# Kernel optimization log

Measured on AMD Instinct MI355X. Metric: run time of the kernel, lower is better.

Reference implementation:

```python
import jax, jax.numpy as jnp
import numpy as np

# Config constants from init_kwargs
DIM_GROUPS = [32, 32]   # hyper_cuts_dim_groups (sum == lsh_key_dim == d_key)
K_MAX = 64              # max candidates kept per query token


def _group_exact_match(qb, kb):
    """qb, kb: [B, L, d] binary {0,1} floats.
    Returns eq[b, i, j] = True iff all d bits of query i equal key j.
    Faithful to merge(Wu-Manber prefix match, Trie full-stride match):
    the Trie stores the full binary vector chunked by stride, so a Trie hit
    requires exact equality of the whole group's bit vector, which subsumes
    the Wu-Manber prefix condition; their intersection is exact equality.
    """
    # number of mismatching bits between query i and key j
    mism = (jnp.einsum('bid,bjd->bij', qb, 1.0 - kb)
            + jnp.einsum('bid,bjd->bij', 1.0 - qb, kb))
    return mism == 0.0


def setup_inputs() -> dict:
    key = jax.random.key(0)
    k1, k2 = jax.random.split(key)
    B, L, D = 4, 2048, 64
    return {
        'query_up': jax.random.normal(k1, (B, L, D), dtype=jnp.float32),
        'key_up': jax.random.normal(k2, (B, L, D), dtype=jnp.float32),
        'head_idx': 0,
    }


def reference(query_up, key_up, head_idx):
    B, L, _ = query_up.shape
    # binary_quantize: (x > 0).float()
    qb = (query_up > 0).astype(jnp.float32)
    kb = (key_up > 0).astype(jnp.float32)
    # per dim-group exact match (Wu-Manber \cap Trie), union across groups
    match = jnp.zeros((B, L, L), dtype=bool)
    start = 0
    for gd in DIM_GROUPS:
        match = match | _group_exact_match(qb[..., start:start + gd],
                                           kb[..., start:start + gd])
        start += gd
    # gather up to K_MAX smallest matching key indices per query, pad with -1
    idx = jnp.where(match, jnp.arange(L, dtype=jnp.int32)[None, None, :], L)
    cand = jnp.sort(idx, axis=-1)[..., :K_MAX]          # [B, L, K_MAX]
    return jnp.where(cand == L, -1, cand)
```

## Files before the change

kernel.cpp:

```cpp
#include <hip/hip_runtime.h>
#include <stdint.h>


#define LSEQ 2048
#define DDIM 64
#define KMAX 64
#define RPW  8
#define MQPB 32

__global__ __launch_bounds__(256) void sig_kernel(
    const float* __restrict__ key, uint2* __restrict__ ksig, int nrows) {
    int wid  = (int)((blockIdx.x * blockDim.x + threadIdx.x) >> 6);
    int lane = threadIdx.x & 63;
    int row0 = wid * RPW;
    if (row0 >= nrows) return;
    const float* base = key + (size_t)row0 * DDIM + lane;
    float v[RPW];
#pragma unroll
    for (int u = 0; u < RPW; ++u)
        v[u] = base[(size_t)u * DDIM];
    unsigned long long m[RPW];
#pragma unroll
    for (int u = 0; u < RPW; ++u)
        m[u] = __ballot(v[u] > 0.0f);
    if (lane == 0) {
#pragma unroll
        for (int u = 0; u < RPW; ++u)
            ksig[row0 + u] = make_uint2((unsigned)m[u], (unsigned)(m[u] >> 32));
    }
}

__global__ __launch_bounds__(1024) void match_kernel(
    const float* __restrict__ query, const uint2* __restrict__ ksig,
    int* __restrict__ out) {
    __shared__ uint4 sh[LSEQ / 2];

    const int bpb = LSEQ / MQPB;
    int b    = blockIdx.x / bpb;
    int qblk = blockIdx.x % bpb;
    int lane = threadIdx.x & 63;
    int wave = threadIdx.x >> 6;

    const uint4* gt = (const uint4*)(ksig + (size_t)b * LSEQ);
    sh[threadIdx.x] = gt[threadIdx.x];

    int q0 = b * LSEQ + qblk * MQPB + wave * 2;
    const float* qp = query + (size_t)q0 * DDIM + lane;
    float v0 = qp[0], v1 = qp[DDIM];
    unsigned long long qm0 = __ballot(v0 > 0.0f);
    unsigned long long qm1 = __ballot(v1 > 0.0f);

    __syncthreads();

    unsigned long long below = (1ull << lane) - 1ull;
    const uint2* ks2 = (const uint2*)sh;
    for (int t = 0; t < 2; ++t) {
        unsigned long long qm = t ? qm1 : qm0;
        unsigned qa = (unsigned)qm, qg = (unsigned)(qm >> 32);
        int* ob = out + (size_t)(q0 + t) * KMAX;

        unsigned long long acc = 0;
        int cnt = 0;
#pragma unroll
        for (int i = 0; i < LSEQ / 128; ++i) {
            uint4 kv = sh[i * 64 + lane];
            bool mA = (kv.x == qa) | (kv.y == qg);
            bool mB = (kv.z == qa) | (kv.w == qg);
            unsigned long long s;
            s = __ballot(mA); acc |= s; cnt += __popcll(s);
            s = __ballot(mB); acc |= s; cnt += __popcll(s);
        }

        if (acc != 0) {
            int c2 = 0;
            for (int c = 0; c < LSEQ / 64; ++c) {
                uint2 kv = ks2[c * 64 + lane];
                bool m = (kv.x == qa) || (kv.y == qg);
                unsigned long long mask = __ballot(m);
                if (m) {
                    int pos = c2 + __popcll(mask & below);
                    if (pos < KMAX) ob[pos] = c * 64 + lane;
                }
                c2 += __popcll(mask);
            }
        }
        if (lane >= cnt) ob[lane] = -1;
    }
}

#define QPB  32
#define NW   16
#define GROUP 32
__global__ __launch_bounds__(1024) void fused_kernel(
    const float* __restrict__ query, const float* __restrict__ key,
    int* __restrict__ out) {
    __shared__ uint2 ks[LSEQ];
    const int bpb  = LSEQ / QPB;
    int b    = blockIdx.x / bpb;
    int qblk = blockIdx.x % bpb;
    int lane = threadIdx.x & 63;
    int wave = threadIdx.x >> 6;
    const float* kb = key + (size_t)b * LSEQ * DDIM;
    for (int g = 0; g < LSEQ / NW / GROUP; ++g) {
        float v[GROUP];
#pragma unroll
        for (int u = 0; u < GROUP; ++u)
            v[u] = kb[(size_t)(g * (NW * GROUP) + u * NW + wave) * DDIM + lane];
        unsigned long long m[GROUP];
#pragma unroll
        for (int u = 0; u < GROUP; ++u) m[u] = __ballot(v[u] > 0.0f);
        if (lane == 0) {
#pragma unroll
            for (int u = 0; u < GROUP; ++u)
                ks[g * (NW * GROUP) + u * NW + wave] =
                    make_uint2((unsigned)m[u], (unsigned)(m[u] >> 32));
        }
    }
    const float* qb = query + ((size_t)b * LSEQ + (size_t)qblk * QPB) * DDIM;
    int q0 = wave * 2;
    float v0 = qb[(size_t)q0 * DDIM + lane];
    float v1 = qb[(size_t)(q0 + 1) * DDIM + lane];
    unsigned long long m0 = __ballot(v0 > 0.0f);
    unsigned long long m1 = __ballot(v1 > 0.0f);
    __syncthreads();
    unsigned long long below = (1ull << lane) - 1ull;
    for (int t = 0; t < 2; ++t) {
        unsigned long long qm = t ? m1 : m0;
        unsigned q1 = (unsigned)qm, q2 = (unsigned)(qm >> 32);
        int* obase = out + ((size_t)b * LSEQ + (size_t)qblk * QPB + q0 + t) * KMAX;
        unsigned long long acc = 0;
        int cnt = 0;
#pragma unroll
        for (int c = 0; c < LSEQ / 64; ++c) {
            uint2 kv = ks[c * 64 + lane];
            bool m = (kv.x == q1) || (kv.y == q2);
            unsigned long long mask = __ballot(m);
            acc |= mask; cnt += __popcll(mask);
        }
        if (acc != 0) {
            int c2 = 0;
            for (int c = 0; c < LSEQ / 64; ++c) {
                uint2 kv = ks[c * 64 + lane];
                bool m = (kv.x == q1) || (kv.y == q2);
                unsigned long long mask = __ballot(m);
                if (m) {
                    int pos = c2 + __popcll(mask & below);
                    if (pos < KMAX) obase[pos] = c * 64 + lane;
                }
                c2 += __popcll(mask);
            }
        }
        if (lane >= cnt) obase[lane] = -1;
    }
}

extern "C" void kernel_launch(void* const* d_in, const int* in_sizes, int n_in,
                              void* d_out, int out_size, void* d_ws, size_t ws_size,
                              hipStream_t stream) {
    const float* q = (const float*)d_in[0];
    const float* k = (const float*)d_in[1];
    int* out = (int*)d_out;

    int total = in_sizes[0];
    int B = total / (LSEQ * DDIM);
    int nrows = B * LSEQ;

    if (ws_size >= (size_t)nrows * sizeof(uint2)) {
        uint2* ksig = (uint2*)d_ws;
        sig_kernel<<<nrows / RPW * 64 / 256, 256, 0, stream>>>(k, ksig, nrows);
        match_kernel<<<nrows / MQPB, 1024, 0, stream>>>(q, ksig, out);
    } else {
        fused_kernel<<<B * (LSEQ / QPB), 1024, 0, stream>>>(q, k, out);
    }
}
```

Baseline: 62.98 us.

## Process four queries per wave to reuse shared-memory key signature loads

Each wave in match_kernel now handles four queries instead of two, and the block shrinks from 1024 to 512 threads. Every uint4 key-signature load from LDS is compared against all four queries in one pass, with a separate ballot per comparison instead of OR-ing before the ballot. The count is no longer gathered in the first pass; it is rebuilt in the write pass, so queries with no match skip that pass entirely. This cuts LDS reads per query and raises per-wave work, but uses more ballots and registers and gives fewer waves per block.

```diff
diff --git a/kernel.cpp b/kernel.cpp
--- a/kernel.cpp
+++ b/kernel.cpp
@@ -7,6 +7,7 @@
 #define KMAX 64
 #define RPW  8
 #define MQPB 32
+#define QPW  4
 
 __global__ __launch_bounds__(256) void sig_kernel(
     const float* __restrict__ key, uint2* __restrict__ ksig, int nrows) {
@@ -30,7 +31,7 @@
     }
 }
 
-__global__ __launch_bounds__(1024) void match_kernel(
+__global__ __launch_bounds__(512) void match_kernel(
     const float* __restrict__ query, const uint2* __restrict__ ksig,
     int* __restrict__ out) {
     __shared__ uint4 sh[LSEQ / 2];
@@ -42,46 +43,51 @@
     int wave = threadIdx.x >> 6;
 
     const uint4* gt = (const uint4*)(ksig + (size_t)b * LSEQ);
-    sh[threadIdx.x] = gt[threadIdx.x];
+    sh[threadIdx.x]       = gt[threadIdx.x];
+    sh[threadIdx.x + 512] = gt[threadIdx.x + 512];
 
-    int q0 = b * LSEQ + qblk * MQPB + wave * 2;
+    int q0 = b * LSEQ + qblk * MQPB + wave * QPW;
     const float* qp = query + (size_t)q0 * DDIM + lane;
-    float v0 = qp[0], v1 = qp[DDIM];
-    unsigned long long qm0 = __ballot(v0 > 0.0f);
-    unsigned long long qm1 = __ballot(v1 > 0.0f);
+    unsigned qa[QPW], qg[QPW];
+#pragma unroll
+    for (int t = 0; t < QPW; ++t) {
+        unsigned long long qm = __ballot(qp[(size_t)t * DDIM] > 0.0f);
+        qa[t] = (unsigned)qm;
+        qg[t] = (unsigned)(qm >> 32);
+    }
 
     __syncthreads();
 
+    unsigned long long acc[QPW] = {};
+#pragma unroll
+    for (int i = 0; i < LSEQ / 128; ++i) {
+        uint4 kv = sh[i * 64 + lane];
+#pragma unroll
+        for (int t = 0; t < QPW; ++t) {
+            unsigned long long sA = __ballot(kv.x == qa[t]);
+            unsigned long long sG = __ballot(kv.y == qg[t]);
+            unsigned long long sB = __ballot(kv.z == qa[t]);
+            unsigned long long sH = __ballot(kv.w == qg[t]);
+            acc[t] |= sA | sG | sB | sH;
+        }
+    }
+
     unsigned long long below = (1ull << lane) - 1ull;
     const uint2* ks2 = (const uint2*)sh;
-    for (int t = 0; t < 2; ++t) {
-        unsigned long long qm = t ? qm1 : qm0;
-        unsigned qa = (unsigned)qm, qg = (unsigned)(qm >> 32);
+#pragma unroll
+    for (int t = 0; t < QPW; ++t) {
         int* ob = out + (size_t)(q0 + t) * KMAX;
-
-        unsigned long long acc = 0;
         int cnt = 0;
-#pragma unroll
-        for (int i = 0; i < LSEQ / 128; ++i) {
-            uint4 kv = sh[i * 64 + lane];
-            bool mA = (kv.x == qa) | (kv.y == qg);
-            bool mB = (kv.z == qa) | (kv.w == qg);
-            unsigned long long s;
-            s = __ballot(mA); acc |= s; cnt += __popcll(s);
-            s = __ballot(mB); acc |= s; cnt += __popcll(s);
-        }
-
-        if (acc != 0) {
-            int c2 = 0;
+        if (acc[t] != 0) {
             for (int c = 0; c < LSEQ / 64; ++c) {
                 uint2 kv = ks2[c * 64 + lane];
-                bool m = (kv.x == qa) || (kv.y == qg);
+                bool m = (kv.x == qa[t]) || (kv.y == qg[t]);
                 unsigned long long mask = __ballot(m);
                 if (m) {
-                    int pos = c2 + __popcll(mask & below);
+                    int pos = cnt + __popcll(mask & below);
                     if (pos < KMAX) ob[pos] = c * 64 + lane;
                 }
-                c2 += __popcll(mask);
+                cnt += __popcll(mask);
             }
         }
         if (lane >= cnt) ob[lane] = -1;
@@ -168,7 +174,7 @@
     if (ws_size >= (size_t)nrows * sizeof(uint2)) {
         uint2* ksig = (uint2*)d_ws;
         sig_kernel<<<nrows / RPW * 64 / 256, 256, 0, stream>>>(k, ksig, nrows);
-        match_kernel<<<nrows / MQPB, 1024, 0, stream>>>(q, ksig, out);
+        match_kernel<<<nrows / MQPB, 512, 0, stream>>>(q, ksig, out);
     } else {
         fused_kernel<<<B * (LSEQ / QPB), 1024, 0, stream>>>(q, k, out);
     }
```

Result: slower. 64.84 us (+3.0%).

## Merge signature and match kernels into one cooperative launch with grid sync

Applied to the files above, without the earlier changes.

Replaces the two-kernel sequence (key signature build, then matching) with a single cooperative kernel. Each block first computes the signatures for its 32 key rows, then a grid-wide barrier makes them visible before the block loads its batch's signatures into shared memory. This removes one kernel launch and the gap between the two kernels, but adds grid-sync overhead and requires all 256 blocks of 1024 threads to be co-resident. If the cooperative launch fails it falls back to the old two-kernel path.

```diff
diff --git a/kernel.cpp b/kernel.cpp
--- a/kernel.cpp
+++ b/kernel.cpp
@@ -1,5 +1,8 @@
 #include <hip/hip_runtime.h>
+#include <hip/hip_cooperative_groups.h>
 #include <stdint.h>
+
+namespace cg = cooperative_groups;
 
 
 #define LSEQ 2048
@@ -8,48 +11,40 @@
 #define RPW  8
 #define MQPB 32
 
-__global__ __launch_bounds__(256) void sig_kernel(
-    const float* __restrict__ key, uint2* __restrict__ ksig, int nrows) {
-    int wid  = (int)((blockIdx.x * blockDim.x + threadIdx.x) >> 6);
-    int lane = threadIdx.x & 63;
-    int row0 = wid * RPW;
-    if (row0 >= nrows) return;
-    const float* base = key + (size_t)row0 * DDIM + lane;
-    float v[RPW];
-#pragma unroll
-    for (int u = 0; u < RPW; ++u)
-        v[u] = base[(size_t)u * DDIM];
-    unsigned long long m[RPW];
-#pragma unroll
-    for (int u = 0; u < RPW; ++u)
-        m[u] = __ballot(v[u] > 0.0f);
-    if (lane == 0) {
-#pragma unroll
-        for (int u = 0; u < RPW; ++u)
-            ksig[row0 + u] = make_uint2((unsigned)m[u], (unsigned)(m[u] >> 32));
-    }
-}
-
-__global__ __launch_bounds__(1024) void match_kernel(
-    const float* __restrict__ query, const uint2* __restrict__ ksig,
-    int* __restrict__ out) {
+__global__ __launch_bounds__(1024) void coop_kernel(
+    const float* __restrict__ query, const float* __restrict__ key,
+    uint2* __restrict__ ksig, int* __restrict__ out) {
     __shared__ uint4 sh[LSEQ / 2];
+
+    int lane = threadIdx.x & 63;
+    int wave = threadIdx.x >> 6;
+
+    int krow = blockIdx.x * 32 + wave * 2;
+    {
+        const float* kp = key + (size_t)krow * DDIM + lane;
+        float k0 = kp[0], k1 = kp[DDIM];
+        unsigned long long km0 = __ballot(k0 > 0.0f);
+        unsigned long long km1 = __ballot(k1 > 0.0f);
+        if (lane == 0)
+            *(uint4*)(ksig + krow) = make_uint4(
+                (unsigned)km0, (unsigned)(km0 >> 32),
+                (unsigned)km1, (unsigned)(km1 >> 32));
+    }
 
     const int bpb = LSEQ / MQPB;
     int b    = blockIdx.x / bpb;
     int qblk = blockIdx.x % bpb;
-    int lane = threadIdx.x & 63;
-    int wave = threadIdx.x >> 6;
-
-    const uint4* gt = (const uint4*)(ksig + (size_t)b * LSEQ);
-    sh[threadIdx.x] = gt[threadIdx.x];
-
     int q0 = b * LSEQ + qblk * MQPB + wave * 2;
     const float* qp = query + (size_t)q0 * DDIM + lane;
     float v0 = qp[0], v1 = qp[DDIM];
     unsigned long long qm0 = __ballot(v0 > 0.0f);
     unsigned long long qm1 = __ballot(v1 > 0.0f);
 
+    __threadfence();
+    cg::this_grid().sync();
+
+    const uint4* gt = (const uint4*)(ksig + (size_t)b * LSEQ);
+    sh[threadIdx.x] = gt[threadIdx.x];
     __syncthreads();
 
     unsigned long long below = (1ull << lane) - 1ull;
@@ -71,6 +66,84 @@
             s = __ballot(mB); acc |= s; cnt += __popcll(s);
         }
 
+        if (acc != 0) {
+            int c2 = 0;
+            for (int c = 0; c < LSEQ / 64; ++c) {
+                uint2 kv = ks2[c * 64 + lane];
+                bool m = (kv.x == qa) || (kv.y == qg);
+                unsigned long long mask = __ballot(m);
+                if (m) {
+                    int pos = c2 + __popcll(mask & below);
+                    if (pos < KMAX) ob[pos] = c * 64 + lane;
+                }
+                c2 += __popcll(mask);
+            }
+        }
+        if (lane >= cnt) ob[lane] = -1;
+    }
+}
+
+__global__ __launch_bounds__(256) void sig_kernel(
+    const float* __restrict__ key, uint2* __restrict__ ksig, int nrows) {
+    int wid  = (int)((blockIdx.x * blockDim.x + threadIdx.x) >> 6);
+    int lane = threadIdx.x & 63;
+    int row0 = wid * RPW;
+    if (row0 >= nrows) return;
+    const float* base = key + (size_t)row0 * DDIM + lane;
+    float v[RPW];
+#pragma unroll
+    for (int u = 0; u < RPW; ++u)
+        v[u] = base[(size_t)u * DDIM];
+    unsigned long long m[RPW];
+#pragma unroll
+    for (int u = 0; u < RPW; ++u)
+        m[u] = __ballot(v[u] > 0.0f);
+    if (lane == 0) {
+#pragma unroll
+        for (int u = 0; u < RPW; ++u)
+            ksig[row0 + u] = make_uint2((unsigned)m[u], (unsigned)(m[u] >> 32));
+    }
+}
+
+__global__ __launch_bounds__(1024) void match_kernel(
+    const float* __restrict__ query, const uint2* __restrict__ ksig,
+    int* __restrict__ out) {
+    __shared__ uint4 sh[LSEQ / 2];
+
+    const int bpb = LSEQ / MQPB;
+    int b    = blockIdx.x / bpb;
+    int qblk = blockIdx.x % bpb;
+    int lane = threadIdx.x & 63;
+    int wave = threadIdx.x >> 6;
+
+    const uint4* gt = (const uint4*)(ksig + (size_t)b * LSEQ);
+    sh[threadIdx.x] = gt[threadIdx.x];
+
+    int q0 = b * LSEQ + qblk * MQPB + wave * 2;
+    const float* qp = query + (size_t)q0 * DDIM + lane;
+    float v0 = qp[0], v1 = qp[DDIM];
+    unsigned long long qm0 = __ballot(v0 > 0.0f);
+    unsigned long long qm1 = __ballot(v1 > 0.0f);
+
+    __syncthreads();
+
+    unsigned long long below = (1ull << lane) - 1ull;
+    const uint2* ks2 = (const uint2*)sh;
+    for (int t = 0; t < 2; ++t) {
+        unsigned long long qm = t ? qm1 : qm0;
+        unsigned qa = (unsigned)qm, qg = (unsigned)(qm >> 32);
+        int* ob = out + (size_t)(q0 + t) * KMAX;
+        unsigned long long acc = 0;
+        int cnt = 0;
+#pragma unroll
+        for (int i = 0; i < LSEQ / 128; ++i) {
+            uint4 kv = sh[i * 64 + lane];
+            bool mA = (kv.x == qa) | (kv.y == qg);
+            bool mB = (kv.z == qa) | (kv.w == qg);
+            unsigned long long s;
+            s = __ballot(mA); acc |= s; cnt += __popcll(s);
+            s = __ballot(mB); acc |= s; cnt += __popcll(s);
+        }
         if (acc != 0) {
             int c2 = 0;
             for (int c = 0; c < LSEQ / 64; ++c) {
@@ -167,8 +240,14 @@
 
     if (ws_size >= (size_t)nrows * sizeof(uint2)) {
         uint2* ksig = (uint2*)d_ws;
-        sig_kernel<<<nrows / RPW * 64 / 256, 256, 0, stream>>>(k, ksig, nrows);
-        match_kernel<<<nrows / MQPB, 1024, 0, stream>>>(q, ksig, out);
+        void* args[] = {(void*)&q, (void*)&k, (void*)&ksig, (void*)&out};
+        hipError_t e = hipLaunchCooperativeKernel(
+            (const void*)coop_kernel, dim3(nrows / MQPB), dim3(1024),
+            args, 0, stream);
+        if (e != hipSuccess) {
+            sig_kernel<<<nrows / RPW * 64 / 256, 256, 0, stream>>>(k, ksig, nrows);
+            match_kernel<<<nrows / MQPB, 1024, 0, stream>>>(q, ksig, out);
+        }
     } else {
         fused_kernel<<<B * (LSEQ / QPB), 1024, 0, stream>>>(q, k, out);
     }
```

New measurement: 161.6 us. 157% more time.
